# Kernel tuning notes

Measured on AMD Instinct MI355X. Metric: run time of the kernel, lower is better.

Reference implementation:

```python
import jax, jax.numpy as jnp
import numpy as np

DIM = 512
HEADS = 8
DIM_HEAD = 64
INNER = HEADS * DIM_HEAD  # 512
SCALE = DIM_HEAD ** -0.5


def setup_inputs() -> dict:
    key = jax.random.key(0)
    k1, k2, k3, k4 = jax.random.split(key, 4)
    x = jax.random.normal(k1, (4, 2048, DIM), dtype=jnp.float32)
    # Dense(inner_dim*3, use_bias=False): weight [dim, 3*inner]
    w_qkv = jax.random.normal(k2, (DIM, 3 * INNER), dtype=jnp.float32) * (DIM ** -0.5)
    # to_out Dense(dim): weight [inner, dim] + bias [dim]
    w_out = jax.random.normal(k3, (INNER, DIM), dtype=jnp.float32) * (INNER ** -0.5)
    b_out = jax.random.normal(k4, (DIM,), dtype=jnp.float32) * 0.01
    return {"x": x, "w_qkv": w_qkv, "w_out": w_out, "b_out": b_out}


def reference(x, w_qkv, w_out, b_out):
    b, n, _ = x.shape
    qkv = x @ w_qkv                                  # [b, n, 3*inner]
    q, k, v = jnp.split(qkv, 3, axis=-1)             # each [b, n, inner]
    def to_heads(t):
        return t.reshape(b, n, HEADS, DIM_HEAD).transpose(0, 2, 1, 3)  # [b, h, n, d]
    q, k, v = map(to_heads, (q, k, v))
    dots = jnp.einsum('bhid,bhjd->bhij', q, k) * SCALE
    attn = jax.nn.softmax(dots, axis=-1)
    out = jnp.einsum('bhij,bhjd->bhid', attn, v)     # [b, h, n, d]
    out = out.transpose(0, 2, 1, 3).reshape(b, n, INNER)
    return out @ w_out + b_out                       # [b, n, dim]
```

## Files before the change

### kernel.cpp

```cpp
#include <hip/hip_runtime.h>
#include <stdint.h>

#define DIM    512
#define HEADS  8
#define DHEAD  64
#define SEQ    2048
#define BATCH  4
#define BH     (BATCH*HEADS)
#define MROWS  (BATCH*SEQ)
#define NQKV   (3*DIM)
#define QSCALE 0.18033688011112042f

typedef __bf16 bf16x8 __attribute__((ext_vector_type(8)));
typedef float  f32x4  __attribute__((ext_vector_type(4)));

typedef unsigned short u16;

#if __has_builtin(__builtin_amdgcn_exp2f)
#define EXP2(x) __builtin_amdgcn_exp2f(x)
#else
#define EXP2(x) exp2f(x)
#endif

__device__ __forceinline__ u16 f2bf(float f) {
    union { float f; uint32_t u; } v; v.f = f;
    uint32_t u = v.u;
    uint32_t r = (u + 0x7FFFu + ((u >> 16) & 1u)) >> 16;
    return (u16)r;
}
__device__ __forceinline__ float bf2f(u16 h) {
    union { uint32_t u; float f; } v; v.u = ((uint32_t)h) << 16;
    return v.f;
}
__device__ __forceinline__ uint32_t pk2bf(float a, float b) {
    union { float f; uint32_t u; } ua, ub; ua.f = a; ub.f = b;
#if __has_builtin(__builtin_amdgcn_perm)
    return __builtin_amdgcn_perm(ub.u + 0x8000u, ua.u + 0x8000u, 0x07060302u);
#else
    return ((ua.u + 0x8000u) >> 16) | ((ub.u + 0x8000u) & 0xFFFF0000u);
#endif
}

__device__ __forceinline__ void async16(const void* g, u16* l) {
    __builtin_amdgcn_global_load_lds(
        (const __attribute__((address_space(1))) void*)g,
        (__attribute__((address_space(3))) void*)l, 16, 0, 0);
}

#define XBLKS  (MROWS * DIM / 4 / 256)
#define WQBLKS (DIM * NQKV / 256)
#define WOBLKS (DIM * DIM / 256)
__global__ void prep(const void* __restrict__ x, const void* __restrict__ wq,
                     const void* __restrict__ wo, u16* __restrict__ xb,
                     u16* __restrict__ wtq, u16* __restrict__ wto,
                     int* __restrict__ flag) {
    __shared__ int cnt;
    int tid = threadIdx.x;
    if (tid == 0) cnt = 0;
    __syncthreads();
    {
        u16 v = ((const u16*)x)[tid * 2];
        int e = (v >> 7) & 0xFF;
        atomicAdd(&cnt, (v == 0) || (e >= 100 && e <= 140));
    }
    __syncthreads();
    int isbf = (cnt >= 192);
    int b = blockIdx.x;
    if (b == 0 && tid == 0) *flag = isbf;

    if (b < XBLKS) {
        int i = b * 256 + tid;
        if (isbf) {
            ((uint2*)xb)[i] = ((const uint2*)x)[i];
        } else {
            float4 v = ((const float4*)x)[i];
            ushort4 o;
            o.x = f2bf(v.x); o.y = f2bf(v.y); o.z = f2bf(v.z); o.w = f2bf(v.w);
            ((ushort4*)xb)[i] = o;
        }
    } else if (b < XBLKS + WQBLKS) {
        int idx = (b - XBLKS) * 256 + tid;
        int k = idx / NQKV, n = idx - k * NQKV;
        u16 v = isbf ? ((const u16*)wq)[idx] : f2bf(((const float*)wq)[idx]);
        wtq[(size_t)n * DIM + k] = v;
    } else {
        int idx = (b - XBLKS - WQBLKS) * 256 + tid;
        int k = idx >> 9, n = idx & 511;
        u16 v = isbf ? ((const u16*)wo)[idx] : f2bf(((const float*)wo)[idx]);
        wto[(size_t)n * DIM + k] = v;
    }
}

template<int KDIM, int TM, int TN>
__device__ __forceinline__ void gemm_lds_db(
        const u16* __restrict__ A, const u16* __restrict__ Bt,
        int m0, int n0, int tid, u16* As, u16* Bs,
        f32x4 (&acc)[TM / 32][TN / 32]) {
    int lane = tid & 63, ln = lane & 15, quad = lane >> 4, w = tid >> 6;
    int wm = (w >> 1) * (TM / 2), wn = (w & 1) * (TN / 2);

    auto stage = [&](int buf, int k0) {
#pragma unroll
        for (int ii = 0; ii < TM / 64; ++ii) {
            int r0 = (ii * 4 + w) * 16;
            int row = r0 + (lane >> 2);
            int seg = (lane & 3) ^ (row & 3);
            async16(A + (size_t)(m0 + row) * KDIM + k0 + seg * 8,
                    As + buf * TM * 32 + r0 * 32);
        }
#pragma unroll
        for (int ii = 0; ii < TN / 64; ++ii) {
            int r0 = (ii * 4 + w) * 16;
            int row = r0 + (lane >> 2);
            int seg = (lane & 3) ^ (row & 3);
            async16(Bt + (size_t)(n0 + row) * KDIM + k0 + seg * 8,
                    Bs + buf * TN * 32 + r0 * 32);
        }
    };

    stage(0, 0);
#pragma unroll 1
    for (int kk = 0; kk < KDIM / 32; ++kk) {
        __syncthreads();
        if (kk + 1 < KDIM / 32) stage((kk + 1) & 1, (kk + 1) * 32);
        const u16* Ac = As + (kk & 1) * TM * 32;
        const u16* Bc = Bs + (kk & 1) * TN * 32;
        bf16x8 a[TM / 32], b[TN / 32];
        int rseg = (quad ^ (ln & 3)) * 8;
#pragma unroll
        for (int i = 0; i < TM / 32; ++i)
            a[i] = *(const bf16x8*)(Ac + (wm + i * 16 + ln) * 32 + rseg);
#pragma unroll
        for (int j = 0; j < TN / 32; ++j)
            b[j] = *(const bf16x8*)(Bc + (wn + j * 16 + ln) * 32 + rseg);
#pragma unroll
        for (int i = 0; i < TM / 32; ++i)
#pragma unroll
            for (int j = 0; j < TN / 32; ++j)
                acc[i][j] = __builtin_amdgcn_mfma_f32_16x16x32_bf16(
                    a[i], b[j], acc[i][j], 0, 0, 0);
    }
}

__global__ __launch_bounds__(256, 3) void qkv_gemm(
        const u16* __restrict__ X, const u16* __restrict__ Wt,
        u16* __restrict__ Qb, u16* __restrict__ Kb, u16* __restrict__ Vt) {
    __shared__ __align__(16) u16 As[2 * 128 * 32];
    __shared__ __align__(16) u16 Bs[2 * 128 * 32];

    int tid  = threadIdx.x;
    int lane = tid & 63, ln = lane & 15, quad = lane >> 4, wid = tid >> 6;
    int m0 = blockIdx.x * 128, n0 = blockIdx.y * 128;
    int wm = (wid >> 1) * 64, wn = (wid & 1) * 64;

    f32x4 acc[4][4];
#pragma unroll
    for (int i = 0; i < 4; ++i)
#pragma unroll
        for (int j = 0; j < 4; ++j) acc[i][j] = 0.f;

    gemm_lds_db<DIM, 128, 128>(X, Wt, m0, n0, tid, As, Bs, acc);

#pragma unroll
    for (int j = 0; j < 4; ++j) {
        int col   = n0 + wn + j * 16 + ln;
        int which = col >> 9;
        int hd    = col & 511;
        int h     = hd >> 6, d = hd & 63;
#pragma unroll
        for (int i = 0; i < 4; ++i) {
            int rbase = m0 + wm + i * 16 + quad * 4;
            if (which == 2) {
                int b = rbase >> 11, n = rbase & 2047;
                int bh = b * HEADS + h;
                uint2 pv;
                pv.x = pk2bf(acc[i][j][0], acc[i][j][1]);
                pv.y = pk2bf(acc[i][j][2], acc[i][j][3]);
                *(uint2*)&Vt[((size_t)bh * DHEAD + d) * SEQ + n] = pv;
            } else {
#pragma unroll
                for (int r = 0; r < 4; ++r) {
                    int row = rbase + r;
                    int b = row >> 11, n = row & 2047;
                    int bh = b * HEADS + h;
                    if (which == 0)
                        Qb[((size_t)bh * SEQ + n) * DHEAD + d] = f2bf(acc[i][j][r] * QSCALE);
                    else
                        Kb[((size_t)bh * SEQ + n) * DHEAD + d] = f2bf(acc[i][j][r]);
                }
            }
        }
    }
}

__global__ __launch_bounds__(256, 2) void flash_attn(
        const u16* __restrict__ Qb, const u16* __restrict__ Kb,
        const u16* __restrict__ Vt, u16* __restrict__ Ob) {
    __shared__ __align__(16) u16 Kc[2][64 * 64];
    __shared__ __align__(16) u16 Vc[2][64 * 64];
    __shared__ __align__(16) u16 Pl[4][32 * 64];

    int tid  = threadIdx.x;
    int lane = tid & 63, ln = lane & 15, quad = lane >> 4, wid = tid >> 6;
    int bh = blockIdx.x;
    int q0 = blockIdx.y * 128 + wid * 32;

    const u16* Qh = Qb + (size_t)bh * SEQ * DHEAD;
    const u16* Kh = Kb + (size_t)bh * SEQ * DHEAD;
    const u16* Vh = Vt + (size_t)bh * DHEAD * SEQ;

    int srow = lane >> 3;
    int gseg = (lane & 7) ^ srow;

    auto stageKV = [&](int buf, int kc) {
#pragma unroll
        for (int ii = 0; ii < 2; ++ii) {
            int slab = wid + ii * 4;
            const u16* gk = Kh + (size_t)(kc + slab * 8 + srow) * DHEAD + gseg * 8;
            async16(gk, &Kc[buf][slab * 8 * 64]);
            const u16* gv = Vh + (size_t)(slab * 8 + srow) * SEQ + kc + gseg * 8;
            async16(gv, &Vc[buf][slab * 8 * 64]);
        }
    };

    bf16x8 qf[2][2];
#pragma unroll
    for (int qt = 0; qt < 2; ++qt)
#pragma unroll
        for (int s = 0; s < 2; ++s)
            qf[qt][s] = *(const bf16x8*)(
                Qh + (size_t)(q0 + qt * 16 + ln) * DHEAD + s * 32 + quad * 8);

    f32x4 o[2][4];
#pragma unroll
    for (int qt = 0; qt < 2; ++qt)
#pragma unroll
        for (int t = 0; t < 4; ++t) o[qt][t] = 0.f;
    float lsum[2] = {0.f, 0.f};

    stageKV(0, 0);
    __syncthreads();

#pragma unroll 1
    for (int kc = 0; kc < SEQ; kc += 64) {
        int cur = (kc >> 6) & 1;
        if (kc + 64 < SEQ) stageKV(cur ^ 1, kc + 64);

        bf16x8 kf[4][2], vf[4][2];
#pragma unroll
        for (int kt = 0; kt < 4; ++kt) {
            int row = kt * 16 + ln;
#pragma unroll
            for (int s = 0; s < 2; ++s) {
                int seg = (s * 4 + quad) ^ (ln & 7);
                kf[kt][s] = *(const bf16x8*)&Kc[cur][row * 64 + seg * 8];
                vf[kt][s] = *(const bf16x8*)&Vc[cur][row * 64 + seg * 8];
            }
        }

        f32x4 st[4][2];
#pragma unroll
        for (int kt = 0; kt < 4; ++kt)
#pragma unroll
            for (int qt = 0; qt < 2; ++qt) st[kt][qt] = 0.f;
#pragma unroll
        for (int kt = 0; kt < 4; ++kt)
#pragma unroll
            for (int qt = 0; qt < 2; ++qt)
#pragma unroll
                for (int s = 0; s < 2; ++s)
                    st[kt][qt] = __builtin_amdgcn_mfma_f32_16x16x32_bf16(
                        kf[kt][s], qf[qt][s], st[kt][qt], 0, 0, 0);

#pragma unroll
        for (int qt = 0; qt < 2; ++qt)
#pragma unroll
            for (int kt = 0; kt < 4; ++kt) {
                float p0 = EXP2(st[kt][qt][0]);
                float p1 = EXP2(st[kt][qt][1]);
                float p2 = EXP2(st[kt][qt][2]);
                float p3 = EXP2(st[kt][qt][3]);
                lsum[qt] += (p0 + p1) + (p2 + p3);
                uint2 d;
                d.x = pk2bf(p0, p1);
                d.y = pk2bf(p2, p3);
                int seg = (kt * 2 + (quad >> 1)) ^ (ln & 7);
                *(uint2*)&Pl[wid][(qt * 16 + ln) * 64 + seg * 8 + (quad & 1) * 4] = d;
            }

        bf16x8 pf[2][2];
#pragma unroll
        for (int qt = 0; qt < 2; ++qt)
#pragma unroll
            for (int s = 0; s < 2; ++s) {
                int seg = (s * 4 + quad) ^ (ln & 7);
                pf[qt][s] = *(const bf16x8*)&Pl[wid][(qt * 16 + ln) * 64 + seg * 8];
            }

#pragma unroll
        for (int t = 0; t < 4; ++t)
#pragma unroll
            for (int s = 0; s < 2; ++s)
#pragma unroll
                for (int qt = 0; qt < 2; ++qt)
                    o[qt][t] = __builtin_amdgcn_mfma_f32_16x16x32_bf16(
                        pf[qt][s], vf[t][s], o[qt][t], 0, 0, 0);

        __syncthreads();
    }

#pragma unroll
    for (int qt = 0; qt < 2; ++qt) {
        float s = lsum[qt];
        s += __shfl_xor(s, 16);
        s += __shfl_xor(s, 32);
        lsum[qt] = 1.0f / s;
    }

    int b = bh >> 3, h = bh & 7;
#pragma unroll
    for (int qt = 0; qt < 2; ++qt) {
#pragma unroll
        for (int t = 0; t < 4; ++t) {
            int d = t * 16 + ln;
#pragma unroll
            for (int r = 0; r < 4; ++r) {
                int qrow = quad * 4 + r;
                float inv = __shfl(lsum[qt], qrow);
                int n = q0 + qt * 16 + qrow;
                Ob[((size_t)(b * SEQ + n)) * DIM + h * DHEAD + d] =
                    f2bf(o[qt][t][r] * inv);
            }
        }
    }
}

__global__ __launch_bounds__(256, 4) void out_gemm(
        const u16* __restrict__ A, const u16* __restrict__ Wt,
        const void* __restrict__ bias, void* __restrict__ out,
        const int* __restrict__ flag) {
    __shared__ __align__(16) u16 As[2 * 64 * 32];
    __shared__ __align__(16) u16 Bs[2 * 64 * 32];

    int tid  = threadIdx.x;
    int lane = tid & 63, ln = lane & 15, quad = lane >> 4, wid = tid >> 6;
    int m0 = blockIdx.x * 64, n0 = blockIdx.y * 64;
    int wm = (wid >> 1) * 32, wn = (wid & 1) * 32;
    int isbf = *flag;

    f32x4 acc[2][2];
#pragma unroll
    for (int i = 0; i < 2; ++i)
#pragma unroll
        for (int j = 0; j < 2; ++j) acc[i][j] = 0.f;

    gemm_lds_db<DIM, 64, 64>(A, Wt, m0, n0, tid, As, Bs, acc);

#pragma unroll
    for (int j = 0; j < 2; ++j) {
        int col = n0 + wn + j * 16 + ln;
        float bv = isbf ? bf2f(((const u16*)bias)[col])
                        : ((const float*)bias)[col];
#pragma unroll
        for (int i = 0; i < 2; ++i) {
            int rbase = m0 + wm + i * 16 + quad * 4;
#pragma unroll
            for (int r = 0; r < 4; ++r) {
                int row = rbase + r;
                size_t off = (size_t)row * DIM + col;
                float val = acc[i][j][r] + bv;
                if (isbf) ((u16*)out)[off] = f2bf(val);
                else      ((float*)out)[off] = val;
            }
        }
    }
}

extern "C" void kernel_launch(void* const* d_in, const int* in_sizes, int n_in,
                              void* d_out, int out_size, void* d_ws, size_t ws_size,
                              hipStream_t stream) {
    const void* x     = d_in[0];
    const void* w_qkv = d_in[1];
    const void* w_out = d_in[2];
    const void* b_out = d_in[3];

    int* flag   = (int*)d_ws;
    u16* x_bf   = (u16*)((char*)d_ws + 16);
    u16* wt_qkv = x_bf + (size_t)MROWS * DIM;
    u16* wt_out = wt_qkv + (size_t)NQKV * DIM;
    u16* Qb     = wt_out + (size_t)DIM * DIM;
    u16* Kb     = Qb + (size_t)BH * SEQ * DHEAD;
    u16* Vt     = Kb + (size_t)BH * SEQ * DHEAD;
    u16* attn   = x_bf;

    prep<<<XBLKS + WQBLKS + WOBLKS, 256, 0, stream>>>(
        x, w_qkv, w_out, x_bf, wt_qkv, wt_out, flag);
    qkv_gemm<<<dim3(MROWS / 128, NQKV / 128), 256, 0, stream>>>(x_bf, wt_qkv, Qb, Kb, Vt);
    flash_attn<<<dim3(BH, SEQ / 128), 256, 0, stream>>>(Qb, Kb, Vt, attn);
    out_gemm<<<dim3(MROWS / 64, DIM / 64), 256, 0, stream>>>(attn, wt_out, b_out, d_out, flag);
}
```

Before: 178.3 us.

## Tile weight transpose via LDS, store Q transposed, widen out_gemm N tile

The prep kernel now transposes weights through a padded 64x64 LDS tile, so global writes are coalesced 16-byte stores instead of scattered 2-byte ones. Q is written head-transposed with packed 8-byte stores, like V, and flash_attn gathers its Q fragments with strided scalar loads. out_gemm moves from 64x64 to 64x128 tiles with fewer blocks and occupancy lowered to 3. The Q read in attention becomes strided but happens only once per block.

Result: no change. 176.2 us (-1.2%).

```diff
diff --git a/kernel.cpp b/kernel.cpp
--- a/kernel.cpp
+++ b/kernel.cpp
@@ -47,14 +47,15 @@
         (__attribute__((address_space(3))) void*)l, 16, 0, 0);
 }
 
-#define XBLKS  (MROWS * DIM / 4 / 256)
-#define WQBLKS (DIM * NQKV / 256)
-#define WOBLKS (DIM * DIM / 256)
+#define XBLKS (MROWS * DIM / 4 / 256)
+#define WQT   ((DIM / 64) * (NQKV / 64))
+#define WOT   ((DIM / 64) * (DIM / 64))
 __global__ void prep(const void* __restrict__ x, const void* __restrict__ wq,
                      const void* __restrict__ wo, u16* __restrict__ xb,
                      u16* __restrict__ wtq, u16* __restrict__ wto,
                      int* __restrict__ flag) {
     __shared__ int cnt;
+    __shared__ __align__(16) u16 tile[64][72];
     int tid = threadIdx.x;
     if (tid == 0) cnt = 0;
     __syncthreads();
@@ -78,16 +79,29 @@
             o.x = f2bf(v.x); o.y = f2bf(v.y); o.z = f2bf(v.z); o.w = f2bf(v.w);
             ((ushort4*)xb)[i] = o;
         }
-    } else if (b < XBLKS + WQBLKS) {
-        int idx = (b - XBLKS) * 256 + tid;
-        int k = idx / NQKV, n = idx - k * NQKV;
-        u16 v = isbf ? ((const u16*)wq)[idx] : f2bf(((const float*)wq)[idx]);
-        wtq[(size_t)n * DIM + k] = v;
-    } else {
-        int idx = (b - XBLKS - WQBLKS) * 256 + tid;
-        int k = idx >> 9, n = idx & 511;
-        u16 v = isbf ? ((const u16*)wo)[idx] : f2bf(((const float*)wo)[idx]);
-        wto[(size_t)n * DIM + k] = v;
+        return;
+    }
+    const void* W; u16* Wt; int N, tb;
+    if (b < XBLKS + WQT) { W = wq; Wt = wtq; N = NQKV; tb = b - XBLKS; }
+    else                 { W = wo; Wt = wto; N = DIM;  tb = b - XBLKS - WQT; }
+    int tn = N / 64;
+    int k0 = (tb / tn) * 64, n0 = (tb - (tb / tn) * tn) * 64;
+
+#pragma unroll 4
+    for (int it = 0; it < 16; ++it) {
+        int idx = it * 256 + tid;
+        int r = idx >> 6, c = idx & 63;
+        u16 v = isbf ? ((const u16*)W)[(size_t)(k0 + r) * N + n0 + c]
+                     : f2bf(((const float*)W)[(size_t)(k0 + r) * N + n0 + c]);
+        tile[c][r] = v;
+    }
+    __syncthreads();
+    {
+        int n = tid >> 2, ks = (tid & 3) * 16;
+        uint4 v0 = *(const uint4*)&tile[n][ks];
+        uint4 v1 = *(const uint4*)&tile[n][ks + 8];
+        *(uint4*)&Wt[(size_t)(n0 + n) * DIM + k0 + ks] = v0;
+        *(uint4*)&Wt[(size_t)(n0 + n) * DIM + k0 + ks + 8] = v1;
     }
 }
 
@@ -144,7 +158,7 @@
 
 __global__ __launch_bounds__(256, 3) void qkv_gemm(
         const u16* __restrict__ X, const u16* __restrict__ Wt,
-        u16* __restrict__ Qb, u16* __restrict__ Kb, u16* __restrict__ Vt) {
+        u16* __restrict__ Qt, u16* __restrict__ Kb, u16* __restrict__ Vt) {
     __shared__ __align__(16) u16 As[2 * 128 * 32];
     __shared__ __align__(16) u16 Bs[2 * 128 * 32];
 
@@ -170,31 +184,26 @@
 #pragma unroll
         for (int i = 0; i < 4; ++i) {
             int rbase = m0 + wm + i * 16 + quad * 4;
-            if (which == 2) {
-                int b = rbase >> 11, n = rbase & 2047;
-                int bh = b * HEADS + h;
+            int b = rbase >> 11, n = rbase & 2047;
+            int bh = b * HEADS + h;
+            if (which == 1) {
+#pragma unroll
+                for (int r = 0; r < 4; ++r)
+                    Kb[((size_t)bh * SEQ + n + r) * DHEAD + d] = f2bf(acc[i][j][r]);
+            } else {
+                float s = (which == 0) ? QSCALE : 1.0f;
                 uint2 pv;
-                pv.x = pk2bf(acc[i][j][0], acc[i][j][1]);
-                pv.y = pk2bf(acc[i][j][2], acc[i][j][3]);
-                *(uint2*)&Vt[((size_t)bh * DHEAD + d) * SEQ + n] = pv;
-            } else {
-#pragma unroll
-                for (int r = 0; r < 4; ++r) {
-                    int row = rbase + r;
-                    int b = row >> 11, n = row & 2047;
-                    int bh = b * HEADS + h;
-                    if (which == 0)
-                        Qb[((size_t)bh * SEQ + n) * DHEAD + d] = f2bf(acc[i][j][r] * QSCALE);
-                    else
-                        Kb[((size_t)bh * SEQ + n) * DHEAD + d] = f2bf(acc[i][j][r]);
-                }
+                pv.x = pk2bf(acc[i][j][0] * s, acc[i][j][1] * s);
+                pv.y = pk2bf(acc[i][j][2] * s, acc[i][j][3] * s);
+                u16* dst = (which == 0) ? Qt : Vt;
+                *(uint2*)&dst[((size_t)bh * DHEAD + d) * SEQ + n] = pv;
             }
         }
     }
 }
 
 __global__ __launch_bounds__(256, 2) void flash_attn(
-        const u16* __restrict__ Qb, const u16* __restrict__ Kb,
+        const u16* __restrict__ Qt, const u16* __restrict__ Kb,
         const u16* __restrict__ Vt, u16* __restrict__ Ob) {
     __shared__ __align__(16) u16 Kc[2][64 * 64];
     __shared__ __align__(16) u16 Vc[2][64 * 64];
@@ -205,7 +214,7 @@
     int bh = blockIdx.x;
     int q0 = blockIdx.y * 128 + wid * 32;
 
-    const u16* Qh = Qb + (size_t)bh * SEQ * DHEAD;
+    const u16* Qh = Qt + (size_t)bh * SEQ * DHEAD;
     const u16* Kh = Kb + (size_t)bh * SEQ * DHEAD;
     const u16* Vh = Vt + (size_t)bh * DHEAD * SEQ;
 
@@ -227,9 +236,13 @@
 #pragma unroll
     for (int qt = 0; qt < 2; ++qt)
 #pragma unroll
-        for (int s = 0; s < 2; ++s)
-            qf[qt][s] = *(const bf16x8*)(
-                Qh + (size_t)(q0 + qt * 16 + ln) * DHEAD + s * 32 + quad * 8);
+        for (int s = 0; s < 2; ++s) {
+            union { u16 a[8]; bf16x8 v; } u;
+#pragma unroll
+            for (int jj = 0; jj < 8; ++jj)
+                u.a[jj] = Qh[(size_t)(s * 32 + quad * 8 + jj) * SEQ + q0 + qt * 16 + ln];
+            qf[qt][s] = u.v;
+        }
 
     f32x4 o[2][4];
 #pragma unroll
@@ -335,29 +348,29 @@
     }
 }
 
-__global__ __launch_bounds__(256, 4) void out_gemm(
+__global__ __launch_bounds__(256, 3) void out_gemm(
         const u16* __restrict__ A, const u16* __restrict__ Wt,
         const void* __restrict__ bias, void* __restrict__ out,
         const int* __restrict__ flag) {
     __shared__ __align__(16) u16 As[2 * 64 * 32];
-    __shared__ __align__(16) u16 Bs[2 * 64 * 32];
+    __shared__ __align__(16) u16 Bs[2 * 128 * 32];
 
     int tid  = threadIdx.x;
     int lane = tid & 63, ln = lane & 15, quad = lane >> 4, wid = tid >> 6;
-    int m0 = blockIdx.x * 64, n0 = blockIdx.y * 64;
-    int wm = (wid >> 1) * 32, wn = (wid & 1) * 32;
+    int m0 = blockIdx.x * 64, n0 = blockIdx.y * 128;
+    int wm = (wid >> 1) * 32, wn = (wid & 1) * 64;
     int isbf = *flag;
 
-    f32x4 acc[2][2];
+    f32x4 acc[2][4];
 #pragma unroll
     for (int i = 0; i < 2; ++i)
 #pragma unroll
-        for (int j = 0; j < 2; ++j) acc[i][j] = 0.f;
-
-    gemm_lds_db<DIM, 64, 64>(A, Wt, m0, n0, tid, As, Bs, acc);
-
-#pragma unroll
-    for (int j = 0; j < 2; ++j) {
+        for (int j = 0; j < 4; ++j) acc[i][j] = 0.f;
+
+    gemm_lds_db<DIM, 64, 128>(A, Wt, m0, n0, tid, As, Bs, acc);
+
+#pragma unroll
+    for (int j = 0; j < 4; ++j) {
         int col = n0 + wn + j * 16 + ln;
         float bv = isbf ? bf2f(((const u16*)bias)[col])
                         : ((const float*)bias)[col];
@@ -388,14 +401,14 @@
     u16* x_bf   = (u16*)((char*)d_ws + 16);
     u16* wt_qkv = x_bf + (size_t)MROWS * DIM;
     u16* wt_out = wt_qkv + (size_t)NQKV * DIM;
-    u16* Qb     = wt_out + (size_t)DIM * DIM;
-    u16* Kb     = Qb + (size_t)BH * SEQ * DHEAD;
+    u16* Qt     = wt_out + (size_t)DIM * DIM;
+    u16* Kb     = Qt + (size_t)BH * SEQ * DHEAD;
     u16* Vt     = Kb + (size_t)BH * SEQ * DHEAD;
     u16* attn   = x_bf;
 
-    prep<<<XBLKS + WQBLKS + WOBLKS, 256, 0, stream>>>(
+    prep<<<XBLKS + WQT + WOT, 256, 0, stream>>>(
         x, w_qkv, w_out, x_bf, wt_qkv, wt_out, flag);
-    qkv_gemm<<<dim3(MROWS / 128, NQKV / 128), 256, 0, stream>>>(x_bf, wt_qkv, Qb, Kb, Vt);
-    flash_attn<<<dim3(BH, SEQ / 128), 256, 0, stream>>>(Qb, Kb, Vt, attn);
-    out_gemm<<<dim3(MROWS / 64, DIM / 64), 256, 0, stream>>>(attn, wt_out, b_out, d_out, flag);
-}
+    qkv_gemm<<<dim3(MROWS / 128, NQKV / 128), 256, 0, stream>>>(x_bf, wt_qkv, Qt, Kb, Vt);
+    flash_attn<<<dim3(BH, SEQ / 128), 256, 0, stream>>>(Qt, Kb, Vt, attn);
+    out_gemm<<<dim3(MROWS / 64, DIM / 128), 256, 0, stream>>>(attn, wt_out, b_out, d_out, flag);
+}
```
